# Optimization experiments

Hardware: AMD Instinct MI355X
Metric: run time of the kernel (lower is better)

## Reference

```python
import jax, jax.numpy as jnp
import numpy as np

NUM_CLASSES = 64


def setup_inputs() -> dict:
    key = jax.random.key(0)
    k1, k2, k3, k4, k5 = jax.random.split(key, 5)
    N, D = 65536, 256
    return {
        "src_feat": jax.random.normal(k1, (N, D), dtype=jnp.float32),
        "trg_feat": jax.random.normal(k2, (N, D), dtype=jnp.float32),
        "src_label": jax.random.randint(k3, (N,), 0, NUM_CLASSES, dtype=jnp.int64),
        "trg_label": jax.random.randint(k4, (N,), 0, NUM_CLASSES, dtype=jnp.int64),
        "trg_feat_un": jax.random.normal(k5, (N, D), dtype=jnp.float32),
    }


def _kl_mean(p_logits, q_logits):
    # torch F.kl_div(log_softmax(p), softmax(q), reduction='mean')
    # = mean over ALL elements of q * (log q - log_softmax(p))
    q = jax.nn.softmax(q_logits, axis=-1)
    logq = jax.nn.log_softmax(q_logits, axis=-1)
    logp = jax.nn.log_softmax(p_logits, axis=-1)
    return jnp.mean(q * (logq - logp))


def reference(src_feat, trg_feat, src_label, trg_label, trg_feat_un):
    C = NUM_CLASSES
    ones_s = jnp.ones(src_feat.shape[0], dtype=src_feat.dtype)
    ones_t = jnp.ones(trg_feat.shape[0], dtype=trg_feat.dtype)
    sum_s = jax.ops.segment_sum(src_feat, src_label, num_segments=C)  # [C,D]
    sum_t = jax.ops.segment_sum(trg_feat, trg_label, num_segments=C)  # [C,D]
    cnt_s = jax.ops.segment_sum(ones_s, src_label, num_segments=C)    # [C]
    cnt_t = jax.ops.segment_sum(ones_t, trg_label, num_segments=C)    # [C]
    u_s = sum_s / cnt_s[:, None]
    u_t = sum_t / cnt_t[:, None]
    u_st = (sum_s + sum_t) / (cnt_s + cnt_t)[:, None]

    feats = jnp.concatenate((src_feat, trg_feat), axis=0)  # [2N, D]
    P_s = feats @ u_s.T    # [2N, C]
    P_t = feats @ u_t.T
    P_st = feats @ u_st.T

    loss_st = (_kl_mean(P_s, P_t) + _kl_mean(P_t, P_s)) / 2
    loss_sst = (_kl_mean(P_s, P_st) + _kl_mean(P_st, P_s)) / 2
    loss_tst = (_kl_mean(P_t, P_st) + _kl_mean(P_st, P_t)) / 2
    return (loss_st + loss_sst + loss_tst) / 3
```

## Files before the change

### kernel.cpp

```cpp
#include <hip/hip_runtime.h>

#define N_ROWS 65536
#define DIMS 256
#define NCLS 64

#define P_SUM_S 0
#define P_SUM_T 131072
#define P_CNT_S 262144
#define P_CNT_T 262656
#define F_SUM_S 263168
#define F_SUM_T 279552
#define ACC_OFF 296064
#define BPACK_OFF 296080

typedef __attribute__((ext_vector_type(8))) short bf16x8;
typedef __attribute__((ext_vector_type(4))) float f32x4;

__device__ __forceinline__ short f2bf(float f) {
  unsigned u = __float_as_uint(f);
  u += 0x7fffu + ((u >> 16) & 1u);
  return (short)(u >> 16);
}

__device__ __forceinline__ float wave_sum64(float v) {
#pragma unroll
  for (int m = 32; m > 0; m >>= 1) v += __shfl_xor(v, m, 64);
  return v;
}
__device__ __forceinline__ float seg_max16(float v) {
#pragma unroll
  for (int m = 8; m > 0; m >>= 1) v = fmaxf(v, __shfl_xor(v, m, 64));
  return v;
}
__device__ __forceinline__ float seg_sum16(float v) {
#pragma unroll
  for (int m = 8; m > 0; m >>= 1) v += __shfl_xor(v, m, 64);
  return v;
}

__global__ __launch_bounds__(256) void seg_sum_kernel(
    const float* __restrict__ src_feat, const float* __restrict__ trg_feat,
    const int* __restrict__ src_label, const int* __restrict__ trg_label,
    float* __restrict__ ws_f) {
  __shared__ float lsum[NCLS * DIMS];
  const int tid = threadIdx.x;
  const bool is_trg = blockIdx.x >= 256;
  const int blk = is_trg ? (blockIdx.x - 256) : blockIdx.x;
  const int part = blockIdx.x & 7;
  const float* feat = is_trg ? trg_feat : src_feat;
  const int* label = is_trg ? trg_label : src_label;
  float* gsum = ws_f + (is_trg ? P_SUM_T : P_SUM_S) + part * 16384;
  float* gcnt = ws_f + (is_trg ? P_CNT_T : P_CNT_S) + part * 64;

  for (int i = tid; i < NCLS * DIMS; i += 256) lsum[i] = 0.f;
  __syncthreads();

  const int row0 = blk * 256;
  float cnt_local = 0.f;
  for (int r = 0; r < 256; r += 8) {
    int lb[8];
    float v[8];
#pragma unroll
    for (int i = 0; i < 8; ++i) {
      lb[i] = label[row0 + r + i];
      v[i] = feat[(size_t)(row0 + r + i) * DIMS + tid];
    }
#pragma unroll
    for (int i = 0; i < 8; ++i) {
      lsum[lb[i] * DIMS + tid] += v[i];
      if (tid < NCLS) cnt_local += (lb[i] == tid) ? 1.f : 0.f;
    }
  }
  __syncthreads();
  for (int c = 0; c < NCLS; ++c)
    atomicAdd(&gsum[c * DIMS + tid], lsum[c * DIMS + tid]);
  if (tid < NCLS) atomicAdd(&gcnt[tid], cnt_local);
}

__global__ __launch_bounds__(256) void reduce_kernel(float* __restrict__ ws_f) {
  const int i = blockIdx.x * 256 + threadIdx.x;
  const int which = i >> 14;
  const int off = i & 16383;
  const float* pp = ws_f + (which ? P_SUM_T : P_SUM_S) + off;
  float s = 0.f;
#pragma unroll
  for (int p = 0; p < 8; ++p) s += pp[p * 16384];
  ws_f[(which ? F_SUM_T : F_SUM_S) + off] = s;
}

__global__ __launch_bounds__(64) void pack_kernel(float* __restrict__ ws_f) {
  const int bx = blockIdx.x;
  const int mat = bx >> 2;
  const int tile = bx & 3;
  const int lane = threadIdx.x;
  const int c = tile * 16 + (lane & 15);

  float cs = 0.f, ct = 0.f;
#pragma unroll
  for (int p = 0; p < 8; ++p) {
    cs += ws_f[P_CNT_S + p * 64 + c];
    ct += ws_f[P_CNT_T + p * 64 + c];
  }

  bf16x8* out = (bf16x8*)(ws_f + BPACK_OFF);
  const float* ss_base = ws_f + F_SUM_S + c * DIMS;
  const float* st_base = ws_f + F_SUM_T + c * DIMS;

#pragma unroll
  for (int s = 0; s < 8; ++s) {
    const int k0 = s * 32 + (lane >> 4) * 8;
    bf16x8 v;
#pragma unroll
    for (int j = 0; j < 8; ++j) {
      const float ss = ss_base[k0 + j];
      const float st = st_base[k0 + j];
      float u;
      if (mat == 0) u = ss / cs;
      else if (mat == 1) u = st / ct;
      else u = (ss + st) / (cs + ct);
      v[j] = f2bf(u);
    }
    out[(bx * 8 + s) * 64 + lane] = v;
  }
}

__global__ __launch_bounds__(256, 2) void main_kernel(
    const float* __restrict__ src_feat, const float* __restrict__ trg_feat,
    const float* __restrict__ ws_f, double* __restrict__ acc_out) {
  const int tid = threadIdx.x;
  const int wave = tid >> 6;
  const int lane = tid & 63;
  const int row0 = blockIdx.x * 128 + wave * 32;
  const float* base = (row0 < N_ROWS)
                          ? src_feat + (size_t)row0 * DIMS
                          : trg_feat + (size_t)(row0 - N_ROWS) * DIMS;
  const float* ap = base + (size_t)((lane & 15) * DIMS + (lane >> 4) * 8);
  const bf16x8* bp = (const bf16x8*)(ws_f + BPACK_OFF);

  f32x4 C[3][4][2];
#pragma unroll
  for (int m = 0; m < 3; ++m)
#pragma unroll
    for (int t = 0; t < 4; ++t)
#pragma unroll
      for (int g = 0; g < 2; ++g) C[m][t][g] = (f32x4){0.f, 0.f, 0.f, 0.f};

#pragma unroll
  for (int s = 0; s < 8; ++s) {
    bf16x8 a[2];
#pragma unroll
    for (int g = 0; g < 2; ++g) {
      const float* p = ap + g * 16 * DIMS + s * 32;
      const float4 lo = *(const float4*)p;
      const float4 hi = *(const float4*)(p + 4);
      bf16x8 t;
      t[0] = f2bf(lo.x); t[1] = f2bf(lo.y); t[2] = f2bf(lo.z); t[3] = f2bf(lo.w);
      t[4] = f2bf(hi.x); t[5] = f2bf(hi.y); t[6] = f2bf(hi.z); t[7] = f2bf(hi.w);
      a[g] = t;
    }
#pragma unroll
    for (int mt = 0; mt < 12; ++mt) {
      const bf16x8 b = bp[(mt * 8 + s) * 64 + lane];
      C[mt >> 2][mt & 3][0] =
          __builtin_amdgcn_mfma_f32_16x16x32_bf16(a[0], b, C[mt >> 2][mt & 3][0], 0, 0, 0);
      C[mt >> 2][mt & 3][1] =
          __builtin_amdgcn_mfma_f32_16x16x32_bf16(a[1], b, C[mt >> 2][mt & 3][1], 0, 0, 0);
    }
  }

  float total = 0.f;
#pragma unroll
  for (int g = 0; g < 2; ++g) {
#pragma unroll
    for (int r = 0; r < 4; ++r) {
      float va[4], vb[4], vc[4];
#pragma unroll
      for (int t = 0; t < 4; ++t) {
        va[t] = C[0][t][g][r];
        vb[t] = C[1][t][g][r];
        vc[t] = C[2][t][g][r];
      }
      float ma = fmaxf(fmaxf(va[0], va[1]), fmaxf(va[2], va[3]));
      float mb = fmaxf(fmaxf(vb[0], vb[1]), fmaxf(vb[2], vb[3]));
      float mc = fmaxf(fmaxf(vc[0], vc[1]), fmaxf(vc[2], vc[3]));
      ma = seg_max16(ma); mb = seg_max16(mb); mc = seg_max16(mc);
      float ea[4], eb[4], ec[4];
      float sa = 0.f, sb = 0.f, sc = 0.f;
#pragma unroll
      for (int t = 0; t < 4; ++t) {
        ea[t] = __expf(va[t] - ma); sa += ea[t];
        eb[t] = __expf(vb[t] - mb); sb += eb[t];
        ec[t] = __expf(vc[t] - mc); sc += ec[t];
      }
      sa = seg_sum16(sa); sb = seg_sum16(sb); sc = seg_sum16(sc);
      const float La = ma + __logf(sa);
      const float Lb = mb + __logf(sb);
      const float Lc = mc + __logf(sc);
      const float isa = 1.f / sa, isb = 1.f / sb, isc = 1.f / sc;
#pragma unroll
      for (int t = 0; t < 4; ++t) {
        const float la = va[t] - La, lb = vb[t] - Lb, lc = vc[t] - Lc;
        const float pa = ea[t] * isa, pb = eb[t] * isb, pc = ec[t] * isc;
        total += pa * ((la - lb) + (la - lc)) + pb * ((lb - la) + (lb - lc)) +
                 pc * ((lc - la) + (lc - lb));
      }
    }
  }
  total = wave_sum64(total);
  if (lane == 0) atomicAdd(acc_out, (double)total);
}

__global__ void finalize_kernel(const double* __restrict__ acc,
                                float* __restrict__ out) {
  out[0] = (float)(acc[0] / 50331648.0);
}

extern "C" void kernel_launch(void* const* d_in, const int* in_sizes, int n_in,
                              void* d_out, int out_size, void* d_ws, size_t ws_size,
                              hipStream_t stream) {
  const float* src_feat = (const float*)d_in[0];
  const float* trg_feat = (const float*)d_in[1];
  const int* src_label = (const int*)d_in[2];
  const int* trg_label = (const int*)d_in[3];
  float* ws_f = (float*)d_ws;
  double* acc = (double*)(ws_f + ACC_OFF);
  float* out = (float*)d_out;

  hipMemsetAsync(d_ws, 0, (size_t)(P_CNT_T + 512) * sizeof(float), stream);
  hipMemsetAsync((void*)acc, 0, sizeof(double), stream);

  seg_sum_kernel<<<512, 256, 0, stream>>>(src_feat, trg_feat, src_label,
                                          trg_label, ws_f);
  reduce_kernel<<<128, 256, 0, stream>>>(ws_f);
  pack_kernel<<<12, 64, 0, stream>>>(ws_f);
  main_kernel<<<1024, 256, 0, stream>>>(src_feat, trg_feat, ws_f, acc);
  finalize_kernel<<<1, 1, 0, stream>>>(acc, out);
}
```

Baseline: 315.3 us.

## Write per-block partial sums, drop memset, stage A tiles in swizzled LDS

The segment-sum kernel now has each wave process its own rows with coalesced float4 loads and LDS atomics. Each block writes its full partial sum to its own workspace slot, which removes the global atomics and the large memset, and the reduce kernel then sums 128 partials per side. The main kernel first loads 32 rows per wave coalesced, converts them to bf16 into an XOR-swizzled LDS tile, and reads MFMA A-fragments from there instead of doing strided global loads. The trade-offs are more partial-buffer traffic (16 MB written and read back), LDS atomic contention, 64 KB of LDS per block in main, which limits occupancy, and removal of the launch_bounds occupancy hint.

New measurement: 454.1 us. 1.44x slower.

```diff
diff --git a/kernel.cpp b/kernel.cpp
--- a/kernel.cpp
+++ b/kernel.cpp
@@ -4,16 +4,15 @@
 #define DIMS 256
 #define NCLS 64
 
-#define P_SUM_S 0
-#define P_SUM_T 131072
-#define P_CNT_S 262144
-#define P_CNT_T 262656
-#define F_SUM_S 263168
-#define F_SUM_T 279552
-#define ACC_OFF 296064
-#define BPACK_OFF 296080
+#define PART_SUM 0
+#define PART_CNT 4194304
+#define F_SUM_S  4210688
+#define F_SUM_T  4227072
+#define BPACK    4243456
+#define ACC_OFF  4268032
 
 typedef __attribute__((ext_vector_type(8))) short bf16x8;
+typedef __attribute__((ext_vector_type(4))) short bf16x4;
 typedef __attribute__((ext_vector_type(4))) float f32x4;
 
 __device__ __forceinline__ short f2bf(float f) {
@@ -43,49 +42,61 @@
     const int* __restrict__ src_label, const int* __restrict__ trg_label,
     float* __restrict__ ws_f) {
   __shared__ float lsum[NCLS * DIMS];
+  __shared__ float lcnt[NCLS];
   const int tid = threadIdx.x;
-  const bool is_trg = blockIdx.x >= 256;
-  const int blk = is_trg ? (blockIdx.x - 256) : blockIdx.x;
-  const int part = blockIdx.x & 7;
+  const int wave = tid >> 6;
+  const int lane = tid & 63;
+  const bool is_trg = blockIdx.x >= 128;
+  const int blk = blockIdx.x & 127;
   const float* feat = is_trg ? trg_feat : src_feat;
   const int* label = is_trg ? trg_label : src_label;
-  float* gsum = ws_f + (is_trg ? P_SUM_T : P_SUM_S) + part * 16384;
-  float* gcnt = ws_f + (is_trg ? P_CNT_T : P_CNT_S) + part * 64;
 
   for (int i = tid; i < NCLS * DIMS; i += 256) lsum[i] = 0.f;
+  if (tid < NCLS) lcnt[tid] = 0.f;
   __syncthreads();
 
-  const int row0 = blk * 256;
-  float cnt_local = 0.f;
-  for (int r = 0; r < 256; r += 8) {
-    int lb[8];
-    float v[8];
-#pragma unroll
-    for (int i = 0; i < 8; ++i) {
-      lb[i] = label[row0 + r + i];
-      v[i] = feat[(size_t)(row0 + r + i) * DIMS + tid];
-    }
-#pragma unroll
-    for (int i = 0; i < 8; ++i) {
-      lsum[lb[i] * DIMS + tid] += v[i];
-      if (tid < NCLS) cnt_local += (lb[i] == tid) ? 1.f : 0.f;
+  const int row0 = blk * 512 + wave * 128;
+  for (int i = 0; i < 128; i += 4) {
+    int lb[4];
+    float4 v[4];
+#pragma unroll
+    for (int j = 0; j < 4; ++j) {
+      const int r = row0 + i + j;
+      lb[j] = label[r];
+      v[j] = ((const float4*)(feat + (size_t)r * DIMS))[lane];
+    }
+#pragma unroll
+    for (int j = 0; j < 4; ++j) {
+      float* p = lsum + lb[j] * DIMS + lane * 4;
+      atomicAdd(p + 0, v[j].x);
+      atomicAdd(p + 1, v[j].y);
+      atomicAdd(p + 2, v[j].z);
+      atomicAdd(p + 3, v[j].w);
+      if (lane == 0) atomicAdd(&lcnt[lb[j]], 1.f);
     }
   }
   __syncthreads();
-  for (int c = 0; c < NCLS; ++c)
-    atomicAdd(&gsum[c * DIMS + tid], lsum[c * DIMS + tid]);
-  if (tid < NCLS) atomicAdd(&gcnt[tid], cnt_local);
+
+  float4* ps = (float4*)(ws_f + PART_SUM + (size_t)blockIdx.x * 16384);
+  const float4* ls = (const float4*)lsum;
+#pragma unroll
+  for (int j = 0; j < 16; ++j) ps[j * 256 + tid] = ls[j * 256 + tid];
+  if (tid < NCLS) ws_f[PART_CNT + blockIdx.x * 64 + tid] = lcnt[tid];
 }
 
 __global__ __launch_bounds__(256) void reduce_kernel(float* __restrict__ ws_f) {
-  const int i = blockIdx.x * 256 + threadIdx.x;
-  const int which = i >> 14;
-  const int off = i & 16383;
-  const float* pp = ws_f + (which ? P_SUM_T : P_SUM_S) + off;
-  float s = 0.f;
-#pragma unroll
-  for (int p = 0; p < 8; ++p) s += pp[p * 16384];
-  ws_f[(which ? F_SUM_T : F_SUM_S) + off] = s;
+  const int id = blockIdx.x * 256 + threadIdx.x;
+  const int side = id >> 12;
+  const int off4 = id & 4095;
+  const float4* p =
+      (const float4*)(ws_f + PART_SUM + (size_t)side * 128 * 16384) + off4;
+  float4 s = make_float4(0.f, 0.f, 0.f, 0.f);
+#pragma unroll 8
+  for (int k = 0; k < 128; ++k) {
+    const float4 v = p[(size_t)k * 4096];
+    s.x += v.x; s.y += v.y; s.z += v.z; s.w += v.w;
+  }
+  ((float4*)(ws_f + (side ? F_SUM_T : F_SUM_S)))[off4] = s;
 }
 
 __global__ __launch_bounds__(64) void pack_kernel(float* __restrict__ ws_f) {
@@ -96,13 +107,12 @@
   const int c = tile * 16 + (lane & 15);
 
   float cs = 0.f, ct = 0.f;
-#pragma unroll
-  for (int p = 0; p < 8; ++p) {
-    cs += ws_f[P_CNT_S + p * 64 + c];
-    ct += ws_f[P_CNT_T + p * 64 + c];
-  }
-
-  bf16x8* out = (bf16x8*)(ws_f + BPACK_OFF);
+  for (int p = 0; p < 128; ++p) {
+    cs += ws_f[PART_CNT + p * 64 + c];
+    ct += ws_f[PART_CNT + (128 + p) * 64 + c];
+  }
+
+  bf16x8* out = (bf16x8*)(ws_f + BPACK);
   const float* ss_base = ws_f + F_SUM_S + c * DIMS;
   const float* st_base = ws_f + F_SUM_T + c * DIMS;
 
@@ -124,9 +134,10 @@
   }
 }
 
-__global__ __launch_bounds__(256, 2) void main_kernel(
+__global__ __launch_bounds__(256) void main_kernel(
     const float* __restrict__ src_feat, const float* __restrict__ trg_feat,
     const float* __restrict__ ws_f, double* __restrict__ acc_out) {
+  __shared__ short tile[4 * 32 * 256];
   const int tid = threadIdx.x;
   const int wave = tid >> 6;
   const int lane = tid & 63;
@@ -134,9 +145,17 @@
   const float* base = (row0 < N_ROWS)
                           ? src_feat + (size_t)row0 * DIMS
                           : trg_feat + (size_t)(row0 - N_ROWS) * DIMS;
-  const float* ap = base + (size_t)((lane & 15) * DIMS + (lane >> 4) * 8);
-  const bf16x8* bp = (const bf16x8*)(ws_f + BPACK_OFF);
-
+  short* my = tile + wave * 8192;
+
+#pragma unroll 8
+  for (int r = 0; r < 32; ++r) {
+    const float4 v = ((const float4*)(base + (size_t)r * DIMS))[lane];
+    bf16x4 pk;
+    pk[0] = f2bf(v.x); pk[1] = f2bf(v.y); pk[2] = f2bf(v.z); pk[3] = f2bf(v.w);
+    *(bf16x4*)(my + r * 256 + ((lane ^ (2 * (r & 15))) * 4)) = pk;
+  }
+
+  const bf16x8* bp = (const bf16x8*)(ws_f + BPACK);
   f32x4 C[3][4][2];
 #pragma unroll
   for (int m = 0; m < 3; ++m)
@@ -150,13 +169,9 @@
     bf16x8 a[2];
 #pragma unroll
     for (int g = 0; g < 2; ++g) {
-      const float* p = ap + g * 16 * DIMS + s * 32;
-      const float4 lo = *(const float4*)p;
-      const float4 hi = *(const float4*)(p + 4);
-      bf16x8 t;
-      t[0] = f2bf(lo.x); t[1] = f2bf(lo.y); t[2] = f2bf(lo.z); t[3] = f2bf(lo.w);
-      t[4] = f2bf(hi.x); t[5] = f2bf(hi.y); t[6] = f2bf(hi.z); t[7] = f2bf(hi.w);
-      a[g] = t;
+      const int rt = g * 16 + (lane & 15);
+      const int c = s * 4 + (lane >> 4);
+      a[g] = *(const bf16x8*)(my + rt * 256 + (c ^ (lane & 15)) * 8);
     }
 #pragma unroll
     for (int mt = 0; mt < 12; ++mt) {
@@ -226,12 +241,11 @@
   double* acc = (double*)(ws_f + ACC_OFF);
   float* out = (float*)d_out;
 
-  hipMemsetAsync(d_ws, 0, (size_t)(P_CNT_T + 512) * sizeof(float), stream);
   hipMemsetAsync((void*)acc, 0, sizeof(double), stream);
 
-  seg_sum_kernel<<<512, 256, 0, stream>>>(src_feat, trg_feat, src_label,
+  seg_sum_kernel<<<256, 256, 0, stream>>>(src_feat, trg_feat, src_label,
                                           trg_label, ws_f);
-  reduce_kernel<<<128, 256, 0, stream>>>(ws_f);
+  reduce_kernel<<<32, 256, 0, stream>>>(ws_f);
   pack_kernel<<<12, 64, 0, stream>>>(ws_f);
   main_kernel<<<1024, 256, 0, stream>>>(src_feat, trg_feat, ws_f, acc);
   finalize_kernel<<<1, 1, 0, stream>>>(acc, out);
```
